# Performance work log

Hardware: AMD Instinct MI355X
Metric: run time of the kernel (lower is better)

The kernel has to match this reference:

```python
import jax, jax.numpy as jnp
import numpy as np
from jax import lax

IMG_SIZE = 640
STRIDES = (8, 16, 32)
NA = 3          # anchors per level
NC = 80         # classes
CONF_THRESH = 0.001
NMS_THRESH = 0.6
ANCHORS = np.array([[10,13],[16,30],[33,23],[30,61],[62,45],[59,119],[116,90],[156,198],[373,326]], np.float32).reshape(3, 3, 2)

def _make_grids():
    gs, st, aw = [], [], []
    for i, s in enumerate(STRIDES):
        hs = ws = IMG_SIZE // s
        gy, gx = np.meshgrid(np.arange(hs), np.arange(ws), indexing='ij')
        gxy = np.stack([gx, gy], -1).astype(np.float32).reshape(1, hs*ws, 1, 2)
        gs.append(gxy)
        st.append(np.full((1, hs*ws, NA, 2), s, np.float32))
        aw.append(np.tile(ANCHORS[i][None], (hs*ws, 1, 1)))
    return (np.concatenate(gs, 1), np.concatenate(st, 1), np.concatenate(aw, 0)[None])

GRID_CELL, STRIDE_T, ANCH_WH = _make_grids()  # [1,HW,1,2], [1,HW,3,2], [1,HW,3,2]

def _nms_classaware(boxes, score, valid):
    # Greedy NMS, class-aware via coordinate offset already applied to boxes.
    # Faithful to the numpy baseline: w,h = max(1e-28, .), areas without +1.
    x1, y1, x2, y2 = boxes[:, 0], boxes[:, 1], boxes[:, 2], boxes[:, 3]
    areas = (x2 - x1) * (y2 - y1)
    order = jnp.argsort(-score)
    N = boxes.shape[0]
    def body(i, state):
        supp, keep = state
        idx = order[i]
        active = jnp.logical_and(jnp.logical_not(supp[idx]), valid[idx])
        keep = keep.at[idx].set(active)
        xx1 = jnp.maximum(x1[idx], x1)
        yy1 = jnp.maximum(y1[idx], y1)
        xx2 = jnp.minimum(x2[idx], x2)
        yy2 = jnp.minimum(y2[idx], y2)
        w = jnp.maximum(1e-28, xx2 - xx1)
        h = jnp.maximum(1e-28, yy2 - yy1)
        inter = w * h
        iou = inter / (areas[idx] + areas - inter)
        newsupp = jnp.logical_and(iou > NMS_THRESH, active)
        newsupp = newsupp.at[idx].set(False)
        return jnp.logical_or(supp, newsupp), keep
    supp0 = jnp.zeros((N,), bool)
    keep0 = jnp.zeros((N,), bool)
    _, keep = lax.fori_loop(0, N, body, (supp0, keep0))
    return keep

def _decode_and_nms(pred_s, pred_m, pred_l):
    objs, clss, regs = [], [], []
    for pred in (pred_s, pred_m, pred_l):
        B, C, H, W = pred.shape
        p = pred.transpose(0, 2, 3, 1).reshape(B, H*W, C)
        objs.append(p[..., :NA].reshape(B, H*W*NA, 1))
        clss.append(p[..., NA:NA*(1+NC)].reshape(B, H*W*NA, NC))
        regs.append(p[..., NA*(1+NC):].reshape(B, H*W, NA, 4))
    obj_pred = jnp.concatenate(objs, axis=1)   # [B, N, 1]
    cls_pred = jnp.concatenate(clss, axis=1)   # [B, N, NC]
    reg_pred = jnp.concatenate(regs, axis=1)   # [B, HW, 3, 4]
    grid = jnp.asarray(GRID_CELL)
    stride = jnp.asarray(STRIDE_T)
    anch = jnp.asarray(ANCH_WH)
    B = reg_pred.shape[0]
    c_xy = (jax.nn.sigmoid(reg_pred[..., :2]) + grid) * stride
    b_wh = jnp.exp(reg_pred[..., 2:]) * anch
    xywh = jnp.concatenate([c_xy, b_wh], -1).reshape(B, -1, 4)
    x1y1 = xywh[..., :2] - xywh[..., 2:] / 2
    x2y2 = xywh[..., :2] + xywh[..., 2:] / 2
    boxes = jnp.clip(jnp.concatenate([x1y1, x2y2], -1) / IMG_SIZE, 0.0, 1.0)[0]  # [N,4]
    obj_s = jax.nn.sigmoid(obj_pred)[0]                     # [N,1]
    scores_all = jax.nn.softmax(cls_pred[0], axis=1) * obj_s  # [N,NC]
    cls_ind = jnp.argmax(scores_all, axis=1)                # [N]
    score = jnp.max(scores_all, axis=1)                     # [N]
    valid = score >= CONF_THRESH
    # class-aware NMS: offset normalized boxes by 2*class so classes never overlap
    boxes_off = boxes + cls_ind[:, None].astype(boxes.dtype) * 2.0
    keep = _nms_classaware(lax.stop_gradient(boxes_off), lax.stop_gradient(score), valid)
    out = jnp.concatenate([
        boxes,                                    # 4 cols
        score[:, None],                           # 1 col
        cls_ind[:, None].astype(boxes.dtype),     # 1 col (non-diff)
        keep[:, None].astype(boxes.dtype),        # 1 col (non-diff)
    ], axis=1)                                    # [N, 7]
    return out

def setup_inputs() -> dict:
    key = jax.random.key(0)
    k1, k2, k3 = jax.random.split(key, 3)
    return {
        'pred_s': jax.random.normal(k1, (1, 255, 80, 80), jnp.float32),
        'pred_m': jax.random.normal(k2, (1, 255, 40, 40), jnp.float32),
        'pred_l': jax.random.normal(k3, (1, 255, 20, 20), jnp.float32),
    }

def reference(pred_s, pred_m, pred_l):
    return _decode_and_nms(pred_s, pred_m, pred_l)
```

## Files before the change

### kernel.cpp

```cpp
#include <hip/hip_runtime.h>
#include <cstdint>

#define NPRED 25200
#define NPOS  8400
#define NCLS  80
#define CAP   512
#define CSTRIDE 16
#define MW    8
#define NCHUNK 132

__device__ __forceinline__ float sigmoidf_(float x) { return 1.0f / (1.0f + expf(-x)); }

__global__ __launch_bounds__(64) void decode_kernel(
    const float* __restrict__ ps, const float* __restrict__ pm, const float* __restrict__ pl,
    float* __restrict__ out, int* __restrict__ counts, float* __restrict__ classbuf)
{
    int chunk = blockIdx.x;
    int a     = blockIdx.y;
    int t     = threadIdx.x;

    const float* p; int HW, W, base, si; float stride; int w0;
    if (chunk < 100)      { p = ps; HW = 6400; W = 80; stride = 8.f;  base = 0;    si = 0; w0 = chunk * 64; }
    else if (chunk < 125) { p = pm; HW = 1600; W = 40; stride = 16.f; base = 6400; si = 1; w0 = (chunk - 100) * 64; }
    else                  { p = pl; HW = 400;  W = 20; stride = 32.f; base = 8000; si = 2; w0 = (chunk - 125) * 64; }

    int local = w0 + t;
    bool valid = local < HW;
    int lclamp = valid ? local : (HW - 1);

    __shared__ float lds[NCLS * 64];

    const float* cbase = p + (size_t)(3 + a * NCLS) * HW;
    int lane_c = t >> 4;
    int j      = (t & 15) << 2;
    int off    = w0 + j; if (off > HW - 4) off = HW - 4;
#pragma unroll
    for (int r0 = 0; r0 < NCLS; r0 += 4) {
        int c = r0 + lane_c;
        float4 v4 = *(const float4*)(cbase + (size_t)c * HW + off);
        *(float4*)&lds[c * 64 + j] = v4;
    }

    float objl = p[(size_t)a * HW + lclamp];
    const float* rb = p + (size_t)(3 + 3 * NCLS + a * 4) * HW + lclamp;
    float tx = rb[0], ty = rb[(size_t)HW], tw = rb[(size_t)2 * HW], th = rb[(size_t)3 * HW];
    __syncthreads();

    float m = -INFINITY;
#pragma unroll 16
    for (int c = 0; c < NCLS; c++) m = fmaxf(m, lds[c * 64 + t]);
    float s = 0.f;
#pragma unroll 16
    for (int c = 0; c < NCLS; c++) {
        float e = expf(lds[c * 64 + t] - m);
        lds[c * 64 + t] = e;
        s += e;
    }
    float obj = sigmoidf_(objl);
    float best = -1.f; int bi = 0;
#pragma unroll 16
    for (int c = 0; c < NCLS; c++) {
        float sc = lds[c * 64 + t] / s * obj;
        if (sc > best) { best = sc; bi = c; }
    }

    if (!valid) return;

    const float AW[9] = {10.f,16.f,33.f, 30.f,62.f,59.f, 116.f,156.f,373.f};
    const float AH[9] = {13.f,30.f,23.f, 61.f,45.f,119.f, 90.f,198.f,326.f};
    float aw = AW[si*3 + a], ah = AH[si*3 + a];

    int y = local / W;
    int x = local - y * W;
    float cx = (sigmoidf_(tx) + (float)x) * stride;
    float cy = (sigmoidf_(ty) + (float)y) * stride;
    float bw = expf(tw) * aw;
    float bh = expf(th) * ah;
    float x1 = fminf(fmaxf((cx - bw / 2.f) / 640.f, 0.f), 1.f);
    float y1 = fminf(fmaxf((cy - bh / 2.f) / 640.f, 0.f), 1.f);
    float x2 = fminf(fmaxf((cx + bw / 2.f) / 640.f, 0.f), 1.f);
    float y2 = fminf(fmaxf((cy + bh / 2.f) / 640.f, 0.f), 1.f);

    int g = (base + local) * 3 + a;
    float clsf = (float)bi;
    float* o = out + (size_t)g * 7;
    o[0] = x1; o[1] = y1; o[2] = x2; o[3] = y2;
    o[4] = best; o[5] = clsf; o[6] = 0.f;

    if (best >= 0.001f) {
        int slot = atomicAdd(&counts[bi * CSTRIDE], 1);
        if (slot < CAP) {
            float off2 = clsf * 2.0f;
            float* r = classbuf + (size_t)(bi * CAP + slot) * 6;
            r[0] = x1 + off2; r[1] = y1 + off2; r[2] = x2 + off2; r[3] = y2 + off2;
            r[4] = best; r[5] = __int_as_float(g);
        }
    }
}

__global__ __launch_bounds__(256) void nms_sort_kernel(
    const int* __restrict__ counts, const float* __restrict__ classbuf,
    float4* __restrict__ g_sbox, int* __restrict__ g_sg)
{
    int c = blockIdx.x;
    int n = counts[c * CSTRIDE]; if (n > CAP) n = CAP;
    int tid = threadIdx.x;

    __shared__ uint64_t key[CAP];
    const float* cls = classbuf + (size_t)c * CAP * 6;

    for (int i = tid; i < n; i += 256) {
        unsigned u = __float_as_uint(cls[i * 6 + 4]);
        u = (u & 0x80000000u) ? ~u : (u | 0x80000000u);
        key[i] = ((uint64_t)(~u) << 15) | (uint64_t)__float_as_int(cls[i * 6 + 5]);
    }
    __syncthreads();

    for (int i = tid; i < n; i += 256) {
        uint64_t k = key[i];
        int r = 0;
        for (int j = 0; j < n; j++) r += (key[j] < k);
        g_sbox[c * CAP + r] = make_float4(cls[i * 6 + 0], cls[i * 6 + 1],
                                          cls[i * 6 + 2], cls[i * 6 + 3]);
        g_sg[c * CAP + r] = (int)(k & 0x7FFF);
    }
}

__global__ __launch_bounds__(256) void nms_build_kernel(
    const int* __restrict__ counts, const float4* __restrict__ g_sbox,
    uint64_t* __restrict__ g_mask)
{
    int c = blockIdx.x;
    int w = blockIdx.y;
    int n = counts[c * CSTRIDE]; if (n > CAP) n = CAP;
    int j0 = w << 6;
    if (j0 >= n) return;
    int j1 = j0 + 64; if (j1 > n) j1 = n;
    int cnt = j1 - j0;
    int tid = threadIdx.x;

    __shared__ float4 sb[64];
    if (tid < cnt) sb[tid] = g_sbox[c * CAP + j0 + tid];
    __syncthreads();

    uint64_t* gm = g_mask + (size_t)c * MW * CAP + (size_t)w * CAP;
    for (int i = tid; i < n; i += 256) {
        float4 b4 = g_sbox[c * CAP + i];
        float Ai = (b4.z - b4.x) * (b4.w - b4.y);
        uint64_t bits = 0;
        if (i + 1 < j1) {
            for (int j = 0; j < cnt; j++) {
                float4 bj = sb[j];
                float xx1 = fmaxf(b4.x, bj.x);
                float yy1 = fmaxf(b4.y, bj.y);
                float xx2 = fminf(b4.z, bj.z);
                float yy2 = fminf(b4.w, bj.w);
                float ww = fmaxf(1e-28f, xx2 - xx1);
                float hh = fmaxf(1e-28f, yy2 - yy1);
                float inter = ww * hh;
                float Aj = (bj.z - bj.x) * (bj.w - bj.y);
                float iou = inter / ((Ai + Aj) - inter);
                if ((j0 + j) > i && iou > 0.6f) bits |= 1ull << j;
            }
        }
        gm[i] = bits;
    }
}

__global__ __launch_bounds__(64) void nms_scan_kernel(
    const int* __restrict__ counts, const int* __restrict__ g_sg,
    const uint64_t* __restrict__ g_mask, float* __restrict__ out)
{
    int c = blockIdx.x;
    int n = counts[c * CSTRIDE]; if (n > CAP) n = CAP;
    int nw = (n + 63) >> 6;
    int lane = threadIdx.x;

    const uint64_t* gm = g_mask + (size_t)c * MW * CAP;
    const int* sg = g_sg + c * CAP;

    uint64_t removed = 0;
    for (int w = 0; w < nw; w++) {
        uint64_t rw = __shfl(removed, w);
        int row = (w << 6) + lane;
        uint64_t diag = (row < n) ? gm[w * CAP + row] : 0ull;
        int rem = n - (w << 6);
        uint64_t valid = (rem >= 64) ? ~0ull : ((1ull << rem) - 1ull);
        uint64_t nulls = __ballot(diag == 0ull);
        uint64_t cand = ~rw & valid;
        uint64_t kw = 0;
        uint64_t it = cand & ~nulls;
        while (it) {
            int b = __ffsll((unsigned long long)it) - 1;
            kw |= 1ull << b;
            uint64_t db = __shfl(diag, b);
            it &= ~db; cand &= ~db;
            it &= ~(1ull << b);
        }
        kw |= cand & nulls;

        int g  = lane >> 3;
        int wp = lane & 7;
        uint64_t acc = 0;
        if (wp < nw) {
            uint64_t mybits = kw & (0xFFull << (g * 8));
            while (mybits) {
                int b = __ffsll((unsigned long long)mybits) - 1;
                mybits &= mybits - 1;
                acc |= gm[wp * CAP + ((w << 6) + b)];
            }
        }
        acc |= __shfl_xor(acc, 8);
        acc |= __shfl_xor(acc, 16);
        acc |= __shfl_xor(acc, 32);
        if (lane < MW) removed |= acc;

        if (row < n && ((kw >> lane) & 1))
            out[(size_t)sg[row] * 7 + 6] = 1.0f;
    }
}

extern "C" void kernel_launch(void* const* d_in, const int* in_sizes, int n_in,
                              void* d_out, int out_size, void* d_ws, size_t ws_size,
                              hipStream_t stream) {
    const float* ps = (const float*)d_in[0];
    const float* pm = (const float*)d_in[1];
    const float* pl = (const float*)d_in[2];
    float* out = (float*)d_out;

    char* ws = (char*)d_ws;
    int*      counts   = (int*)ws;
    float*    classbuf = (float*)(ws + 8192);
    int*      g_sg     = (int*)(ws + 8192 + 983040);
    float4*   g_sbox   = (float4*)(ws + 8192 + 983040 + 163840);
    uint64_t* g_mask   = (uint64_t*)(ws + 8192 + 983040 + 163840 + 655360);

    hipMemsetAsync(counts, 0, 8192, stream);
    decode_kernel<<<dim3(NCHUNK, 3), 64, 0, stream>>>(ps, pm, pl, out, counts, classbuf);
    nms_sort_kernel<<<NCLS, 256, 0, stream>>>(counts, classbuf, g_sbox, g_sg);
    nms_build_kernel<<<dim3(NCLS, MW), 256, 0, stream>>>(counts, g_sbox, g_mask);
    nms_scan_kernel<<<NCLS, 64, 0, stream>>>(counts, g_sg, g_mask, out);
}
```

Baseline: 119.4 us.

## Precompute sort keys in decode, split rank sort across blocks, pad NMS tiles

```diff
diff --git a/kernel.cpp b/kernel.cpp
--- a/kernel.cpp
+++ b/kernel.cpp
@@ -13,7 +13,8 @@
 
 __global__ __launch_bounds__(64) void decode_kernel(
     const float* __restrict__ ps, const float* __restrict__ pm, const float* __restrict__ pl,
-    float* __restrict__ out, int* __restrict__ counts, float* __restrict__ classbuf)
+    float* __restrict__ out, int* __restrict__ counts,
+    float4* __restrict__ g_boxin, uint64_t* __restrict__ g_key)
 {
     int chunk = blockIdx.x;
     int a     = blockIdx.y;
@@ -34,16 +35,17 @@
     int lane_c = t >> 4;
     int j      = (t & 15) << 2;
     int off    = w0 + j; if (off > HW - 4) off = HW - 4;
+
+    float4 vreg[20];
 #pragma unroll
-    for (int r0 = 0; r0 < NCLS; r0 += 4) {
-        int c = r0 + lane_c;
-        float4 v4 = *(const float4*)(cbase + (size_t)c * HW + off);
-        *(float4*)&lds[c * 64 + j] = v4;
-    }
-
+    for (int r0 = 0; r0 < 20; r0++)
+        vreg[r0] = *(const float4*)(cbase + (size_t)(r0 * 4 + lane_c) * HW + off);
     float objl = p[(size_t)a * HW + lclamp];
     const float* rb = p + (size_t)(3 + 3 * NCLS + a * 4) * HW + lclamp;
     float tx = rb[0], ty = rb[(size_t)HW], tw = rb[(size_t)2 * HW], th = rb[(size_t)3 * HW];
+#pragma unroll
+    for (int r0 = 0; r0 < 20; r0++)
+        *(float4*)&lds[(r0 * 4 + lane_c) * 64 + j] = vreg[r0];
     __syncthreads();
 
     float m = -INFINITY;
@@ -91,37 +93,54 @@
         int slot = atomicAdd(&counts[bi * CSTRIDE], 1);
         if (slot < CAP) {
             float off2 = clsf * 2.0f;
-            float* r = classbuf + (size_t)(bi * CAP + slot) * 6;
-            r[0] = x1 + off2; r[1] = y1 + off2; r[2] = x2 + off2; r[3] = y2 + off2;
-            r[4] = best; r[5] = __int_as_float(g);
+            g_boxin[bi * CAP + slot] = make_float4(x1 + off2, y1 + off2,
+                                                   x2 + off2, y2 + off2);
+            unsigned u = __float_as_uint(best);
+            u = (u & 0x80000000u) ? ~u : (u | 0x80000000u);
+            g_key[bi * CAP + slot] = ((uint64_t)(~u) << 15) | (uint64_t)g;
         }
     }
 }
 
 __global__ __launch_bounds__(256) void nms_sort_kernel(
-    const int* __restrict__ counts, const float* __restrict__ classbuf,
-    float4* __restrict__ g_sbox, int* __restrict__ g_sg)
-{
-    int c = blockIdx.x;
+    const int* __restrict__ counts, const uint64_t* __restrict__ g_key,
+    const float4* __restrict__ g_boxin, float4* __restrict__ g_sbox,
+    int* __restrict__ g_sg)
+{
+    int c  = blockIdx.x;
+    int i0 = blockIdx.y << 6;
     int n = counts[c * CSTRIDE]; if (n > CAP) n = CAP;
+    if (i0 >= n) return;
     int tid = threadIdx.x;
 
     __shared__ uint64_t key[CAP];
-    const float* cls = classbuf + (size_t)c * CAP * 6;
-
-    for (int i = tid; i < n; i += 256) {
-        unsigned u = __float_as_uint(cls[i * 6 + 4]);
-        u = (u & 0x80000000u) ? ~u : (u | 0x80000000u);
-        key[i] = ((uint64_t)(~u) << 15) | (uint64_t)__float_as_int(cls[i * 6 + 5]);
-    }
+    for (int i = tid; i < n; i += 256) key[i] = g_key[c * CAP + i];
     __syncthreads();
 
-    for (int i = tid; i < n; i += 256) {
-        uint64_t k = key[i];
-        int r = 0;
-        for (int j = 0; j < n; j++) r += (key[j] < k);
-        g_sbox[c * CAP + r] = make_float4(cls[i * 6 + 0], cls[i * 6 + 1],
-                                          cls[i * 6 + 2], cls[i * 6 + 3]);
+    int item = i0 + (tid >> 2);
+    int sub  = tid & 3;
+    bool act = item < n;
+    int r = 0;
+    uint64_t k = 0;
+    if (act) {
+        k = key[item];
+        int nq = (n + 3) >> 2;
+        int lo = sub * nq; if (lo > n) lo = n;
+        int hi = lo + nq;  if (hi > n) hi = n;
+        int jj = lo;
+        for (; jj + 8 <= hi; jj += 8) {
+            int t0 = key[jj]   < k, t1 = key[jj+1] < k;
+            int t2 = key[jj+2] < k, t3 = key[jj+3] < k;
+            int t4 = key[jj+4] < k, t5 = key[jj+5] < k;
+            int t6 = key[jj+6] < k, t7 = key[jj+7] < k;
+            r += t0 + t1 + t2 + t3 + t4 + t5 + t6 + t7;
+        }
+        for (; jj < hi; jj++) r += (key[jj] < k);
+    }
+    r += __shfl_xor(r, 1);
+    r += __shfl_xor(r, 2);
+    if (act && sub == 0) {
+        g_sbox[c * CAP + r] = g_boxin[c * CAP + item];
         g_sg[c * CAP + r] = (int)(k & 0x7FFF);
     }
 }
@@ -140,7 +159,11 @@
     int tid = threadIdx.x;
 
     __shared__ float4 sb[64];
-    if (tid < cnt) sb[tid] = g_sbox[c * CAP + j0 + tid];
+    if (tid < 64) {
+        float4 sv = make_float4(3e30f, 3e30f, 3e30f, 3e30f);
+        if (tid < cnt) sv = g_sbox[c * CAP + j0 + tid];
+        sb[tid] = sv;
+    }
     __syncthreads();
 
     uint64_t* gm = g_mask + (size_t)c * MW * CAP + (size_t)w * CAP;
@@ -149,8 +172,9 @@
         float Ai = (b4.z - b4.x) * (b4.w - b4.y);
         uint64_t bits = 0;
         if (i + 1 < j1) {
-            for (int j = 0; j < cnt; j++) {
-                float4 bj = sb[j];
+#pragma unroll 8
+            for (int jq = 0; jq < 64; jq++) {
+                float4 bj = sb[jq];
                 float xx1 = fmaxf(b4.x, bj.x);
                 float yy1 = fmaxf(b4.y, bj.y);
                 float xx2 = fminf(b4.z, bj.z);
@@ -160,7 +184,7 @@
                 float inter = ww * hh;
                 float Aj = (bj.z - bj.x) * (bj.w - bj.y);
                 float iou = inter / ((Ai + Aj) - inter);
-                if ((j0 + j) > i && iou > 0.6f) bits |= 1ull << j;
+                if ((j0 + jq) > i && iou > 0.6f) bits |= 1ull << jq;
             }
         }
         gm[i] = bits;
@@ -229,15 +253,16 @@
     float* out = (float*)d_out;
 
     char* ws = (char*)d_ws;
-    int*      counts   = (int*)ws;
-    float*    classbuf = (float*)(ws + 8192);
-    int*      g_sg     = (int*)(ws + 8192 + 983040);
-    float4*   g_sbox   = (float4*)(ws + 8192 + 983040 + 163840);
-    uint64_t* g_mask   = (uint64_t*)(ws + 8192 + 983040 + 163840 + 655360);
+    int*      counts  = (int*)ws;
+    float4*   g_boxin = (float4*)(ws + 8192);
+    uint64_t* g_key   = (uint64_t*)(ws + 663552);
+    float4*   g_sbox  = (float4*)(ws + 991232);
+    int*      g_sg    = (int*)(ws + 1646592);
+    uint64_t* g_mask  = (uint64_t*)(ws + 1810432);
 
     hipMemsetAsync(counts, 0, 8192, stream);
-    decode_kernel<<<dim3(NCHUNK, 3), 64, 0, stream>>>(ps, pm, pl, out, counts, classbuf);
-    nms_sort_kernel<<<NCLS, 256, 0, stream>>>(counts, classbuf, g_sbox, g_sg);
+    decode_kernel<<<dim3(NCHUNK, 3), 64, 0, stream>>>(ps, pm, pl, out, counts, g_boxin, g_key);
+    nms_sort_kernel<<<dim3(NCLS, MW), 256, 0, stream>>>(counts, g_key, g_boxin, g_sbox, g_sg);
     nms_build_kernel<<<dim3(NCLS, MW), 256, 0, stream>>>(counts, g_sbox, g_mask);
     nms_scan_kernel<<<NCLS, 64, 0, stream>>>(counts, g_sg, g_mask, out);
 }
```

Measured after the change: 111.4 us. 6.7% less time.
